# Kernel optimization log

Hardware: AMD Instinct MI355X
Metric: run time of the kernel (lower is better)

## Reference

```python
import jax, jax.numpy as jnp
import numpy as np

N_NODES = 50000
N_EDGES = 800000
D = 128


def setup_inputs() -> dict:
    key = jax.random.key(0)
    ks = jax.random.split(key, 8)
    scale = 1.0 / np.sqrt(D)
    x = jax.random.normal(ks[0], (N_NODES, D), dtype=jnp.float32)
    edge_index = jax.random.randint(ks[1], (2, N_EDGES), 0, N_NODES, dtype=jnp.int64)
    return {
        "x": x,
        "edge_index": edge_index,
        "w1_l": jax.random.normal(ks[2], (D, D), dtype=jnp.float32) * scale,
        "w1_r": jax.random.normal(ks[3], (D, D), dtype=jnp.float32) * scale,
        "b1": jnp.zeros((D,), dtype=jnp.float32),
        "w2_l": jax.random.normal(ks[4], (D, D), dtype=jnp.float32) * scale,
        "w2_r": jax.random.normal(ks[5], (D, D), dtype=jnp.float32) * scale,
        "b2": jnp.zeros((D,), dtype=jnp.float32),
    }


def _sage_conv(x, src, dst, w_l, w_r, b):
    # mean aggregation of source features at destination nodes
    n = x.shape[0]
    msg = x[src]                                            # [E, D] gather
    agg = jax.ops.segment_sum(msg, dst, num_segments=n)      # [N, D] scatter-add
    cnt = jax.ops.segment_sum(jnp.ones((src.shape[0],), x.dtype), dst, num_segments=n)
    mean = agg / jnp.maximum(cnt, 1.0)[:, None]
    # out = lin_l(mean_agg) + lin_r(x) + bias  (PyG SAGEConv default)
    return mean @ w_l.T + x @ w_r.T + b


def reference(x, edge_index, w1_l, w1_r, b1, w2_l, w2_r, b2):
    src, dst = edge_index[0], edge_index[1]
    h = jax.nn.relu(_sage_conv(x, src, dst, w1_l, w1_r, b1))
    out = _sage_conv(h, src, dst, w2_l, w2_r, b2)
    return out
```

## Files before the change

kernel.cpp:

```cpp
#include <hip/hip_runtime.h>

#define D 128
#define CAP 48
#define TILE 32

typedef unsigned short u16;
typedef unsigned int u32;
typedef _Float16 f16;
typedef __attribute__((ext_vector_type(4))) _Float16 h4;
typedef __attribute__((ext_vector_type(8))) _Float16 h8;
typedef __attribute__((ext_vector_type(4))) float f32x4;

__global__ __launch_bounds__(256) void mega_prep(const float* __restrict__ x,
                                                 f16* __restrict__ xh, int n8,
                                                 const float* __restrict__ w1l,
                                                 const float* __restrict__ w1r,
                                                 const float* __restrict__ w2l,
                                                 const float* __restrict__ w2r,
                                                 f16* __restrict__ wb1,
                                                 f16* __restrict__ wb2,
                                                 const int* __restrict__ src,
                                                 const int* __restrict__ dst,
                                                 int* __restrict__ cnt,
                                                 int* __restrict__ edge_pad,
                                                 int E, int bucketDiv, int perChunk,
                                                 int cvtBlocks, int wBlocks) {
    const int b = blockIdx.x;
    const int t = threadIdx.x;
    if (b < cvtBlocks) {
        int i = b * 256 + t;
        if (i < n8) {
            float4 v0 = reinterpret_cast<const float4*>(x)[2 * i];
            float4 v1 = reinterpret_cast<const float4*>(x)[2 * i + 1];
            h8 o;
            o[0] = (f16)v0.x; o[1] = (f16)v0.y; o[2] = (f16)v0.z; o[3] = (f16)v0.w;
            o[4] = (f16)v1.x; o[5] = (f16)v1.y; o[6] = (f16)v1.z; o[7] = (f16)v1.w;
            reinterpret_cast<h8*>(xh)[i] = o;
        }
    } else if (b < cvtBlocks + wBlocks) {
        int e = (b - cvtBlocks) * 256 + t;
        int which = e >> 15;
        int i = e & 32767;
        int j = i >> 8, k = i & 255;
        const float* wl = which ? w2l : w1l;
        const float* wr = which ? w2r : w1r;
        f16* wb = which ? wb2 : wb1;
        float v = (k < 128) ? wl[j * 128 + k] : wr[j * 128 + k - 128];
        wb[i] = (f16)v;
    } else {
        const int fillIdx = b - cvtBlocks - wBlocks;
        const int bucket = b & 7;
        const int chunk = fillIdx >> 3;
        const int lo = bucket * bucketDiv;
        const int hi = lo + bucketDiv;
        const int beg = chunk * perChunk;
        const int end = min(E, beg + perChunk);
        for (int base = beg + t * 4; base < end; base += 1024) {
            if (base + 3 < end) {
                int4 d = *reinterpret_cast<const int4*>(dst + base);
                if (d.x >= lo && d.x < hi) { int p = atomicAdd(&cnt[d.x], 1); if (p < CAP) edge_pad[d.x * CAP + p] = src[base + 0]; }
                if (d.y >= lo && d.y < hi) { int p = atomicAdd(&cnt[d.y], 1); if (p < CAP) edge_pad[d.y * CAP + p] = src[base + 1]; }
                if (d.z >= lo && d.z < hi) { int p = atomicAdd(&cnt[d.z], 1); if (p < CAP) edge_pad[d.z * CAP + p] = src[base + 2]; }
                if (d.w >= lo && d.w < hi) { int p = atomicAdd(&cnt[d.w], 1); if (p < CAP) edge_pad[d.w * CAP + p] = src[base + 3]; }
            } else {
                for (int j = 0; j < 4 && base + j < end; ++j) {
                    int d = dst[base + j];
                    if (d >= lo && d < hi) { int p = atomicAdd(&cnt[d], 1); if (p < CAP) edge_pad[d * CAP + p] = src[base + j]; }
                }
            }
        }
    }
}

template <int RELU, int OUTF16>
__global__ __launch_bounds__(256) void sage_fused(const f16* __restrict__ feat,
                                                  const int* __restrict__ cnt,
                                                  const int* __restrict__ edge_pad,
                                                  const f16* __restrict__ wb,
                                                  const float* __restrict__ bias,
                                                  float* __restrict__ outf,
                                                  f16* __restrict__ outh, int n) {
    __shared__ f16 sM[TILE * 128];
    __shared__ int eLds[TILE * CAP];
    __shared__ int degLds[TILE];
    const int t = threadIdx.x;
    const int base = blockIdx.x * TILE;
    char* sMb = reinterpret_cast<char*>(sM);

    {
        const int4* gseg = reinterpret_cast<const int4*>(edge_pad + (size_t)base * CAP);
#pragma unroll
        for (int i = 0; i < (TILE * CAP / 4 + 255) / 256; ++i) {
            int idx = i * 256 + t;
            if (idx < TILE * CAP / 4) reinterpret_cast<int4*>(eLds)[idx] = gseg[idx];
        }
        if (t < TILE) degLds[t] = (base + t < n) ? cnt[base + t] : 0;
    }
    __syncthreads();

    {
        const int halfId = t >> 5;
        const int lane = t & 31;
#pragma unroll
        for (int rnd = 0; rnd < TILE / 8; ++rnd) {
            const int nl = rnd * 8 + halfId;
            const int deg = degLds[nl];
            const int stored = min(deg, CAP);
            const int* ep = &eLds[nl * CAP];

            h4 acc = (h4){0, 0, 0, 0};
            int j = 0;
            for (; j + 8 <= stored; j += 8) {
                int4 ia = *reinterpret_cast<const int4*>(ep + j);
                int4 ib = *reinterpret_cast<const int4*>(ep + j + 4);
                h4 v0 = *reinterpret_cast<const h4*>(feat + (size_t)ia.x * D + lane * 4);
                h4 v1 = *reinterpret_cast<const h4*>(feat + (size_t)ia.y * D + lane * 4);
                h4 v2 = *reinterpret_cast<const h4*>(feat + (size_t)ia.z * D + lane * 4);
                h4 v3 = *reinterpret_cast<const h4*>(feat + (size_t)ia.w * D + lane * 4);
                h4 v4 = *reinterpret_cast<const h4*>(feat + (size_t)ib.x * D + lane * 4);
                h4 v5 = *reinterpret_cast<const h4*>(feat + (size_t)ib.y * D + lane * 4);
                h4 v6 = *reinterpret_cast<const h4*>(feat + (size_t)ib.z * D + lane * 4);
                h4 v7 = *reinterpret_cast<const h4*>(feat + (size_t)ib.w * D + lane * 4);
                acc += ((v0 + v1) + (v2 + v3)) + ((v4 + v5) + (v6 + v7));
            }
            for (; j + 4 <= stored; j += 4) {
                int4 ia = *reinterpret_cast<const int4*>(ep + j);
                h4 v0 = *reinterpret_cast<const h4*>(feat + (size_t)ia.x * D + lane * 4);
                h4 v1 = *reinterpret_cast<const h4*>(feat + (size_t)ia.y * D + lane * 4);
                h4 v2 = *reinterpret_cast<const h4*>(feat + (size_t)ia.z * D + lane * 4);
                h4 v3 = *reinterpret_cast<const h4*>(feat + (size_t)ia.w * D + lane * 4);
                acc += (v0 + v1) + (v2 + v3);
            }
            for (; j < stored; ++j) {
                int s = ep[j];
                acc += *reinterpret_cast<const h4*>(feat + (size_t)s * D + lane * 4);
            }

            const f16 sc = (deg > 0) ? (f16)(1.f / (float)deg) : (f16)0;
            h4 o = acc * (h4){sc, sc, sc, sc};
            int lin = nl * 256 + lane * 8;
            *reinterpret_cast<h4*>(sMb + (lin ^ ((nl & 7) << 4))) = o;
        }
    }
    __syncthreads();

    const int wid = t >> 6, lane = t & 63;
    const int l15 = lane & 15, l4 = lane >> 4;
    const int colBase = wid * 32;

    int rowA[2];
#pragma unroll
    for (int m = 0; m < 2; ++m) {
        int r = base + m * 16 + l15;
        rowA[m] = (r < n) ? r : 0;
    }

    f32x4 acc2[2][2];
#pragma unroll
    for (int m = 0; m < 2; ++m)
#pragma unroll
        for (int q = 0; q < 2; ++q) acc2[m][q] = (f32x4){0.f, 0.f, 0.f, 0.f};

    const int swr = (l15 & 7) << 4;

#pragma unroll
    for (int ks = 0; ks < 8; ++ks) {
        h8 afr[2];
        if (ks < 4) {
#pragma unroll
            for (int m = 0; m < 2; ++m) {
                int lin = (m * 16 + l15) * 256 + ks * 64 + l4 * 16;
                afr[m] = *reinterpret_cast<const h8*>(sMb + (lin ^ swr));
            }
        } else {
            const int kk = (ks & 3) * 32 + l4 * 8;
#pragma unroll
            for (int m = 0; m < 2; ++m)
                afr[m] = *reinterpret_cast<const h8*>(feat + (size_t)rowA[m] * D + kk);
        }
#pragma unroll
        for (int q = 0; q < 2; ++q) {
            h8 bfr = *reinterpret_cast<const h8*>(
                wb + (size_t)(colBase + q * 16 + l15) * 256 + ks * 32 + l4 * 8);
#pragma unroll
            for (int m = 0; m < 2; ++m)
                acc2[m][q] = __builtin_amdgcn_mfma_f32_16x16x32_f16(afr[m], bfr, acc2[m][q], 0, 0, 0);
        }
    }

#pragma unroll
    for (int q = 0; q < 2; ++q) {
        const int col = colBase + q * 16 + l15;
        const float bv = bias[col];
#pragma unroll
        for (int m = 0; m < 2; ++m) {
#pragma unroll
            for (int r = 0; r < 4; ++r) {
                int orow = base + m * 16 + l4 * 4 + r;
                if (orow < n) {
                    float v = acc2[m][q][r] + bv;
                    if (RELU) v = fmaxf(v, 0.f);
                    if (OUTF16)
                        outh[(size_t)orow * D + col] = (f16)v;
                    else
                        outf[(size_t)orow * D + col] = v;
                }
            }
        }
    }
}

extern "C" void kernel_launch(void* const* d_in, const int* in_sizes, int n_in,
                              void* d_out, int out_size, void* d_ws, size_t ws_size,
                              hipStream_t stream) {
    const float* x   = (const float*)d_in[0];
    const int*   ei  = (const int*)d_in[1];
    const float* w1l = (const float*)d_in[2];
    const float* w1r = (const float*)d_in[3];
    const float* b1  = (const float*)d_in[4];
    const float* w2l = (const float*)d_in[5];
    const float* w2r = (const float*)d_in[6];
    const float* b2  = (const float*)d_in[7];
    float* out = (float*)d_out;

    const int N = in_sizes[0] / D;
    const int E = in_sizes[1] / 2;

    const int* src = ei;
    const int* dst = ei + E;

    const int gridFused = (N + TILE - 1) / TILE;
    const int Nceil = gridFused * TILE;

    char* ws = (char*)d_ws;
    auto align = [](size_t v) { return (v + 255) & ~(size_t)255; };
    const size_t featB = align((size_t)N * D * sizeof(f16));

    f16* xh       = (f16*)ws;   ws += featB;
    f16* hh       = (f16*)ws;   ws += featB;
    f16* wb1      = (f16*)ws;   ws += align(128 * 256 * sizeof(f16));
    f16* wb2      = (f16*)ws;   ws += align(128 * 256 * sizeof(f16));
    int* cnt      = (int*)ws;   ws += align((size_t)Nceil * sizeof(int));
    int* edge_pad = (int*)ws;   ws += align((size_t)Nceil * CAP * sizeof(int));

    const int n8        = N * D / 8;
    const int cvtBlocks = (n8 + 255) / 256;
    const int wBlocks   = 256;
    const int bucketDiv = (N + 7) / 8;
    const int perChunk  = 5120;
    const int chunks    = (E + perChunk - 1) / perChunk;
    const int fillBlocks = 8 * chunks;

    hipMemsetAsync(cnt, 0, (size_t)Nceil * sizeof(int), stream);
    mega_prep<<<cvtBlocks + wBlocks + fillBlocks, 256, 0, stream>>>(
        x, xh, n8, w1l, w1r, w2l, w2r, wb1, wb2,
        src, dst, cnt, edge_pad, E, bucketDiv, perChunk, cvtBlocks, wBlocks);

    sage_fused<1, 1><<<gridFused, 256, 0, stream>>>(xh, cnt, edge_pad, wb1, b1, nullptr, hh, N);

    sage_fused<0, 0><<<gridFused, 256, 0, stream>>>(hh, cnt, edge_pad, wb2, b2, out, nullptr, N);
}
```

Baseline: 152.6 us.

## Split edge fill into separate kernel and stage outputs through LDS for coalesced stores

The memset of the count array moves into the prep kernel as zeroing blocks, and the edge bucketing fill becomes its own kernel launched afterwards. That kernel loads src as int4 alongside dst and uses size_t indexing. The fused SAGE kernel now writes its MFMA results to shared memory, which reuses the aggregation buffer, and then stores them to global as full 16-byte rows instead of scattered scalar stores. This adds a kernel launch and extra barriers and shared-memory traffic in exchange for coalesced output writes and one fewer memset call.

```diff
diff --git a/kernel.cpp b/kernel.cpp
--- a/kernel.cpp
+++ b/kernel.cpp
@@ -4,27 +4,21 @@
 #define CAP 48
 #define TILE 32
 
-typedef unsigned short u16;
-typedef unsigned int u32;
 typedef _Float16 f16;
 typedef __attribute__((ext_vector_type(4))) _Float16 h4;
 typedef __attribute__((ext_vector_type(8))) _Float16 h8;
 typedef __attribute__((ext_vector_type(4))) float f32x4;
 
-__global__ __launch_bounds__(256) void mega_prep(const float* __restrict__ x,
-                                                 f16* __restrict__ xh, int n8,
-                                                 const float* __restrict__ w1l,
-                                                 const float* __restrict__ w1r,
-                                                 const float* __restrict__ w2l,
-                                                 const float* __restrict__ w2r,
-                                                 f16* __restrict__ wb1,
-                                                 f16* __restrict__ wb2,
-                                                 const int* __restrict__ src,
-                                                 const int* __restrict__ dst,
-                                                 int* __restrict__ cnt,
-                                                 int* __restrict__ edge_pad,
-                                                 int E, int bucketDiv, int perChunk,
-                                                 int cvtBlocks, int wBlocks) {
+__global__ __launch_bounds__(256) void prep_kernel(const float* __restrict__ x,
+                                                   f16* __restrict__ xh, int n8,
+                                                   const float* __restrict__ w1l,
+                                                   const float* __restrict__ w1r,
+                                                   const float* __restrict__ w2l,
+                                                   const float* __restrict__ w2r,
+                                                   f16* __restrict__ wb1,
+                                                   f16* __restrict__ wb2,
+                                                   int* __restrict__ cnt, int Nceil,
+                                                   int cvtBlocks, int wBlocks) {
     const int b = blockIdx.x;
     const int t = threadIdx.x;
     if (b < cvtBlocks) {
@@ -48,25 +42,34 @@
         float v = (k < 128) ? wl[j * 128 + k] : wr[j * 128 + k - 128];
         wb[i] = (f16)v;
     } else {
-        const int fillIdx = b - cvtBlocks - wBlocks;
-        const int bucket = b & 7;
-        const int chunk = fillIdx >> 3;
-        const int lo = bucket * bucketDiv;
-        const int hi = lo + bucketDiv;
-        const int beg = chunk * perChunk;
-        const int end = min(E, beg + perChunk);
-        for (int base = beg + t * 4; base < end; base += 1024) {
-            if (base + 3 < end) {
-                int4 d = *reinterpret_cast<const int4*>(dst + base);
-                if (d.x >= lo && d.x < hi) { int p = atomicAdd(&cnt[d.x], 1); if (p < CAP) edge_pad[d.x * CAP + p] = src[base + 0]; }
-                if (d.y >= lo && d.y < hi) { int p = atomicAdd(&cnt[d.y], 1); if (p < CAP) edge_pad[d.y * CAP + p] = src[base + 1]; }
-                if (d.z >= lo && d.z < hi) { int p = atomicAdd(&cnt[d.z], 1); if (p < CAP) edge_pad[d.z * CAP + p] = src[base + 2]; }
-                if (d.w >= lo && d.w < hi) { int p = atomicAdd(&cnt[d.w], 1); if (p < CAP) edge_pad[d.w * CAP + p] = src[base + 3]; }
-            } else {
-                for (int j = 0; j < 4 && base + j < end; ++j) {
-                    int d = dst[base + j];
-                    if (d >= lo && d < hi) { int p = atomicAdd(&cnt[d], 1); if (p < CAP) edge_pad[d * CAP + p] = src[base + j]; }
-                }
+        int i = (b - cvtBlocks - wBlocks) * 256 + t;
+        if (i < Nceil) cnt[i] = 0;
+    }
+}
+
+__global__ __launch_bounds__(256) void fill_pad_xcd(const int* __restrict__ src,
+                                                    const int* __restrict__ dst,
+                                                    int* __restrict__ cnt,
+                                                    int* __restrict__ edge_pad,
+                                                    int E, int bucketDiv, int perChunk) {
+    const int b = blockIdx.x & 7;
+    const int chunk = blockIdx.x >> 3;
+    const int lo = b * bucketDiv;
+    const int hi = lo + bucketDiv;
+    const int beg = chunk * perChunk;
+    const int end = min(E, beg + perChunk);
+    for (int base = beg + threadIdx.x * 4; base < end; base += 1024) {
+        if (base + 3 < end) {
+            int4 d = *reinterpret_cast<const int4*>(dst + base);
+            int4 s = *reinterpret_cast<const int4*>(src + base);
+            if (d.x >= lo && d.x < hi) { int p = atomicAdd(&cnt[d.x], 1); if (p < CAP) edge_pad[(size_t)d.x * CAP + p] = s.x; }
+            if (d.y >= lo && d.y < hi) { int p = atomicAdd(&cnt[d.y], 1); if (p < CAP) edge_pad[(size_t)d.y * CAP + p] = s.y; }
+            if (d.z >= lo && d.z < hi) { int p = atomicAdd(&cnt[d.z], 1); if (p < CAP) edge_pad[(size_t)d.z * CAP + p] = s.z; }
+            if (d.w >= lo && d.w < hi) { int p = atomicAdd(&cnt[d.w], 1); if (p < CAP) edge_pad[(size_t)d.w * CAP + p] = s.w; }
+        } else {
+            for (int j = 0; j < 4 && base + j < end; ++j) {
+                int d = dst[base + j];
+                if (d >= lo && d < hi) { int p = atomicAdd(&cnt[d], 1); if (p < CAP) edge_pad[(size_t)d * CAP + p] = src[base + j]; }
             }
         }
     }
@@ -80,12 +83,12 @@
                                                   const float* __restrict__ bias,
                                                   float* __restrict__ outf,
                                                   f16* __restrict__ outh, int n) {
-    __shared__ f16 sM[TILE * 128];
-    __shared__ int eLds[TILE * CAP];
-    __shared__ int degLds[TILE];
+    __shared__ float4 smemRaw4[1024];
+    char* sMb   = reinterpret_cast<char*>(smemRaw4);
+    int*  eLds  = reinterpret_cast<int*>(sMb + 8192);
+    int*  degLds= reinterpret_cast<int*>(sMb + 8192 + 6144);
     const int t = threadIdx.x;
     const int base = blockIdx.x * TILE;
-    char* sMb = reinterpret_cast<char*>(sM);
 
     {
         const int4* gseg = reinterpret_cast<const int4*>(edge_pad + (size_t)base * CAP);
@@ -188,24 +191,56 @@
         }
     }
 
-#pragma unroll
-    for (int q = 0; q < 2; ++q) {
-        const int col = colBase + q * 16 + l15;
-        const float bv = bias[col];
-#pragma unroll
-        for (int m = 0; m < 2; ++m) {
-#pragma unroll
-            for (int r = 0; r < 4; ++r) {
-                int orow = base + m * 16 + l4 * 4 + r;
-                if (orow < n) {
+    __syncthreads();
+    if (OUTF16) {
+        f16* oT = reinterpret_cast<f16*>(sMb);
+#pragma unroll
+        for (int q = 0; q < 2; ++q) {
+            const int col = colBase + q * 16 + l15;
+            const float bv = bias[col];
+#pragma unroll
+            for (int m = 0; m < 2; ++m)
+#pragma unroll
+                for (int r = 0; r < 4; ++r) {
                     float v = acc2[m][q][r] + bv;
                     if (RELU) v = fmaxf(v, 0.f);
-                    if (OUTF16)
-                        outh[(size_t)orow * D + col] = (f16)v;
-                    else
-                        outf[(size_t)orow * D + col] = v;
+                    oT[(m * 16 + l4 * 4 + r) * 128 + col] = (f16)v;
                 }
-            }
+        }
+        __syncthreads();
+#pragma unroll
+        for (int it = 0; it < 2; ++it) {
+            int idx = it * 256 + t;
+            int row = idx >> 4;
+            int c = (idx & 15) * 8;
+            if (base + row < n)
+                *reinterpret_cast<h8*>(outh + (size_t)(base + row) * D + c) =
+                    *reinterpret_cast<const h8*>(oT + row * 128 + c);
+        }
+    } else {
+        float* oT = reinterpret_cast<float*>(sMb);
+#pragma unroll
+        for (int q = 0; q < 2; ++q) {
+            const int col = colBase + q * 16 + l15;
+            const float bv = bias[col];
+#pragma unroll
+            for (int m = 0; m < 2; ++m)
+#pragma unroll
+                for (int r = 0; r < 4; ++r) {
+                    float v = acc2[m][q][r] + bv;
+                    if (RELU) v = fmaxf(v, 0.f);
+                    oT[(m * 16 + l4 * 4 + r) * 128 + col] = v;
+                }
+        }
+        __syncthreads();
+#pragma unroll
+        for (int it = 0; it < 4; ++it) {
+            int idx = it * 256 + t;
+            int row = idx >> 5;
+            int c = (idx & 31) * 4;
+            if (base + row < n)
+                *reinterpret_cast<float4*>(outf + (size_t)(base + row) * D + c) =
+                    *reinterpret_cast<const float4*>(oT + row * 128 + c);
         }
     }
 }
@@ -246,15 +281,15 @@
     const int n8        = N * D / 8;
     const int cvtBlocks = (n8 + 255) / 256;
     const int wBlocks   = 256;
+    const int zBlocks   = (Nceil + 255) / 256;
     const int bucketDiv = (N + 7) / 8;
     const int perChunk  = 5120;
     const int chunks    = (E + perChunk - 1) / perChunk;
-    const int fillBlocks = 8 * chunks;
-
-    hipMemsetAsync(cnt, 0, (size_t)Nceil * sizeof(int), stream);
-    mega_prep<<<cvtBlocks + wBlocks + fillBlocks, 256, 0, stream>>>(
-        x, xh, n8, w1l, w1r, w2l, w2r, wb1, wb2,
-        src, dst, cnt, edge_pad, E, bucketDiv, perChunk, cvtBlocks, wBlocks);
+
+    prep_kernel<<<cvtBlocks + wBlocks + zBlocks, 256, 0, stream>>>(
+        x, xh, n8, w1l, w1r, w2l, w2r, wb1, wb2, cnt, Nceil, cvtBlocks, wBlocks);
+
+    fill_pad_xcd<<<8 * chunks, 256, 0, stream>>>(src, dst, cnt, edge_pad, E, bucketDiv, perChunk);
 
     sage_fused<1, 1><<<gridFused, 256, 0, stream>>>(xh, cnt, edge_pad, wb1, b1, nullptr, hh, N);
 
```

New measurement: 141.5 us. 7.3% less time.
